# Kernel optimization log

Hardware: AMD Instinct MI355X
Metric: run time of the kernel (lower is better)

Reference implementation:

```python
import jax, jax.numpy as jnp
import numpy as np
import math

B, S, D, H, DFF, E, TOPK = 2, 2048, 768, 12, 3072, 8, 2
DH = D // H
EPS = 1e-5


def _ln(x, g, b):
    mu = jnp.mean(x, axis=-1, keepdims=True)
    var = jnp.mean(jnp.square(x - mu), axis=-1, keepdims=True)
    return (x - mu) * jax.lax.rsqrt(var + EPS) * g + b


def _router(x, rw, rb):
    # x: [B,S,D] -> probs [B,S,E], topk indices [B,S,K]
    logits = jnp.einsum('bsd,de->bse', x, rw) + rb
    probs = jax.nn.softmax(logits, axis=-1)
    topv, topi = jax.lax.top_k(probs, TOPK)
    return probs, topv, topi


def setup_inputs() -> dict:
    key = jax.random.key(0)
    ks = jax.random.split(key, 12)
    s = 0.02
    inp = {
        'x': jax.random.normal(ks[0], (B, S, D), dtype=jnp.float32),
        'wq': jax.random.normal(ks[1], (D, D), dtype=jnp.float32) * s,
        'bq': jnp.zeros((D,), jnp.float32),
        'wk': jax.random.normal(ks[2], (D, D), dtype=jnp.float32) * s,
        'bk': jnp.zeros((D,), jnp.float32),
        'wv': jax.random.normal(ks[3], (D, D), dtype=jnp.float32) * s,
        'bv': jnp.zeros((D,), jnp.float32),
        'wo': jax.random.normal(ks[4], (D, D), dtype=jnp.float32) * s,
        'bo': jnp.zeros((D,), jnp.float32),
        'norm1_g': jnp.ones((D,), jnp.float32),
        'norm1_b': jnp.zeros((D,), jnp.float32),
        'router_w': jax.random.normal(ks[5], (D, E), dtype=jnp.float32) * s,
        'router_b': jnp.zeros((E,), jnp.float32),
        'ew1': jax.random.normal(ks[6], (E, D, DFF), dtype=jnp.float32) * s,
        'eb1': jnp.zeros((E, DFF), jnp.float32),
        'ew2': jax.random.normal(ks[7], (E, DFF, D), dtype=jnp.float32) * s,
        'eb2': jnp.zeros((E, D), jnp.float32),
        'norm2_g': jnp.ones((D,), jnp.float32),
        'norm2_b': jnp.zeros((D,), jnp.float32),
    }
    return inp


def reference(x, wq, bq, wk, bk, wv, bv, wo, bo,
              norm1_g, norm1_b, router_w, router_b,
              ew1, eb1, ew2, eb2, norm2_g, norm2_b):
    # ---- multi-head self-attention ----
    def proj(w, b):
        return (jnp.einsum('bsd,de->bse', x, w) + b).reshape(B, S, H, DH).transpose(0, 2, 1, 3)
    q, k, v = proj(wq, bq), proj(wk, bk), proj(wv, bv)
    scores = jnp.einsum('bhqd,bhkd->bhqk', q, k) / math.sqrt(DH)
    attn = jax.nn.softmax(scores, axis=-1)
    ctx = jnp.einsum('bhqk,bhkd->bhqd', attn, v).transpose(0, 2, 1, 3).reshape(B, S, D)
    attn_out = jnp.einsum('bsd,de->bse', ctx, wo) + bo
    x1 = _ln(x + attn_out, norm1_g, norm1_b)

    # ---- MoE: top-k routing with renormalized gates ----
    probs, topv, topi = _router(x1, router_w, router_b)
    gates = topv / jnp.sum(topv, axis=-1, keepdims=True)          # [B,S,K]
    # combine weights per expert: [B,S,E]
    combine = jnp.sum(jax.nn.one_hot(topi, E, dtype=x1.dtype) * gates[..., None], axis=-2)
    moe_out = jnp.zeros_like(x1)
    for e in range(E):  # fixed small expert count
        h = jax.nn.relu(jnp.einsum('bsd,df->bsf', x1, ew1[e]) + eb1[e])
        y = jnp.einsum('bsf,fd->bsd', h, ew2[e]) + eb2[e]
        moe_out = moe_out + combine[..., e:e + 1] * y
    x2 = _ln(x1 + moe_out, norm2_g, norm2_b)

    # ---- redundant second router call + load-balancing aux loss ----
    probs2, _, topi2 = _router(x2, router_w, router_b)
    mask2 = jax.nn.one_hot(topi2, E, dtype=x2.dtype)              # [B,S,K,E]
    frac = jnp.mean(mask2, axis=(0, 1, 2))                        # fraction routed per expert
    prob = jnp.mean(probs2, axis=(0, 1))                          # mean router prob per expert
    aux_loss = E * jnp.sum(frac * prob)
    return (x2, aux_loss)
```

## Files before the change

### kernel.cpp

```cpp
#include <hip/hip_runtime.h>

typedef _Float16 f16;
typedef _Float16 f16x8 __attribute__((ext_vector_type(8)));
typedef _Float16 f16x4v __attribute__((ext_vector_type(4)));
typedef float f32x4 __attribute__((ext_vector_type(4)));

#define THREADS 256
#define BM 128
#define BN 128
#define BKK 64

#define WSCALE 256.0f
#define WDESCALE (1.0f/256.0f)

static __device__ __forceinline__ float wred_sum(float x){
#pragma unroll
  for (int o = 32; o; o >>= 1) x += __shfl_xor(x, o);
  return x;
}
static __device__ __forceinline__ int wred_sumi(int x){
#pragma unroll
  for (int o = 32; o; o >>= 1) x += __shfl_xor(x, o);
  return x;
}
static __device__ __forceinline__ float bred_sum(float x){
  __shared__ float r[4];
  x = wred_sum(x);
  if ((threadIdx.x & 63) == 0) r[threadIdx.x >> 6] = x;
  __syncthreads();
  float s = r[0] + r[1] + r[2] + r[3];
  __syncthreads();
  return s;
}

template<class Epi>
static __device__ __forceinline__ void gemm_core(const f16* A, const f16* BT,
                                                 int m0, int K, int N, int n0, Epi epi)
{
  __shared__ __align__(16) f16 Al[BM][BKK];
  __shared__ __align__(16) f16 Bl[BN][BKK];
  const int t = threadIdx.x;
  const int lane = t & 63, wave = t >> 6;
  const int wr = wave >> 1, wc = wave & 1;

  const f16* gA[4];
  const f16* gB[4];
#pragma unroll
  for (int i = 0; i < 4; ++i) {
    int c = i * THREADS + t;
    int r = c >> 3;
    int kc = (((c & 7) ^ (r & 7)) << 3);
    gA[i] = A + (size_t)(m0 + r) * K + kc;
    gB[i] = BT + (size_t)(n0 + r) * K + kc;
  }

  f32x4 acc[4][4];
#pragma unroll
  for (int i = 0; i < 4; ++i)
#pragma unroll
    for (int j = 0; j < 4; ++j)
#pragma unroll
      for (int r = 0; r < 4; ++r) acc[i][j][r] = 0.0f;

  f16* Als = &Al[0][0];
  f16* Bls = &Bl[0][0];

  for (int k0 = 0; k0 < K; k0 += BKK) {
    __syncthreads();
#pragma unroll
    for (int i = 0; i < 4; ++i) {
      int c = i * THREADS + t;
      __builtin_amdgcn_global_load_lds(
          (const __attribute__((address_space(1))) void*)(gA[i] + k0),
          (__attribute__((address_space(3))) void*)(Als + (size_t)c * 8), 16, 0, 0);
      __builtin_amdgcn_global_load_lds(
          (const __attribute__((address_space(1))) void*)(gB[i] + k0),
          (__attribute__((address_space(3))) void*)(Bls + (size_t)c * 8), 16, 0, 0);
    }
    __syncthreads();
#pragma unroll
    for (int kk = 0; kk < BKK; kk += 32) {
      const int lrow = lane & 15, lk = (lane >> 4) * 8;
      const int sx = (lrow & 7) << 3;
      f16x8 af[4], bf[4];
#pragma unroll
      for (int mf = 0; mf < 4; ++mf)
        af[mf] = *(const f16x8*)&Als[(size_t)(wr * 64 + mf * 16 + lrow) * BKK + ((kk + lk) ^ sx)];
#pragma unroll
      for (int nf = 0; nf < 4; ++nf)
        bf[nf] = *(const f16x8*)&Bls[(size_t)(wc * 64 + nf * 16 + lrow) * BKK + ((kk + lk) ^ sx)];
#pragma unroll
      for (int mf = 0; mf < 4; ++mf)
#pragma unroll
        for (int nf = 0; nf < 4; ++nf)
          acc[mf][nf] = __builtin_amdgcn_mfma_f32_16x16x32_f16(af[mf], bf[nf], acc[mf][nf], 0, 0, 0);
    }
  }
  const int lr4 = (lane >> 4) * 4, lc = lane & 15;
#pragma unroll
  for (int mf = 0; mf < 4; ++mf)
#pragma unroll
    for (int nf = 0; nf < 4; ++nf)
#pragma unroll
      for (int r = 0; r < 4; ++r) {
        int row = wr * 64 + mf * 16 + lr4 + r;
        int col = n0 + wc * 64 + nf * 16 + lc;
        epi(row, col, acc[mf][nf][r]);
      }
}

__global__ __launch_bounds__(256) void k_cvt(const float* x, f16* o){
  size_t i = (size_t)blockIdx.x * 256 + threadIdx.x;
  float4 v = ((const float4*)x)[i];
  f16x4v h;
  h[0] = (f16)v.x; h[1] = (f16)v.y; h[2] = (f16)v.z; h[3] = (f16)v.w;
  *(f16x4v*)(o + i * 4) = h;
}

__global__ __launch_bounds__(256) void k_transpose(const float* in, f16* out, int Kd, int Nd){
  __shared__ float tl[64][65];
  const float* ip = in + (size_t)blockIdx.z * Kd * Nd;
  f16* op = out + (size_t)blockIdx.z * Kd * Nd;
  int n0 = blockIdx.x * 64, k0 = blockIdx.y * 64;
  int tx = threadIdx.x & 15, ty = threadIdx.x >> 4;
#pragma unroll
  for (int j = 0; j < 64; j += 16) {
    float4 v = *(const float4*)(ip + (size_t)(k0 + ty + j) * Nd + n0 + tx * 4);
    tl[ty + j][tx * 4 + 0] = v.x;
    tl[ty + j][tx * 4 + 1] = v.y;
    tl[ty + j][tx * 4 + 2] = v.z;
    tl[ty + j][tx * 4 + 3] = v.w;
  }
  __syncthreads();
#pragma unroll
  for (int j = 0; j < 64; j += 16) {
    f16x4v h;
    h[0] = (f16)(tl[tx * 4 + 0][ty + j] * WSCALE);
    h[1] = (f16)(tl[tx * 4 + 1][ty + j] * WSCALE);
    h[2] = (f16)(tl[tx * 4 + 2][ty + j] * WSCALE);
    h[3] = (f16)(tl[tx * 4 + 3][ty + j] * WSCALE);
    *(f16x4v*)(op + (size_t)(n0 + ty + j) * Kd + k0 + tx * 4) = h;
  }
}

__global__ __launch_bounds__(256) void k_gemm_qkv(const f16* xb,
    const f16* wqT, const f16* wkT, const f16* wvT,
    const float* bq, const float* bk, const float* bv,
    f16* Q, f16* Ko, f16* V)
{
  int m0 = blockIdx.x * 128, n0 = blockIdx.y * 128, z = blockIdx.z;
  const f16* BT = (z == 0) ? wqT : ((z == 1) ? wkT : wvT);
  const float* bias = (z == 0) ? bq : ((z == 1) ? bk : bv);
  auto epi = [&](int row, int col, float vv) {
    int grow = m0 + row;
    int b = grow >> 11, s = grow & 2047;
    int h = col >> 6, dh = col & 63;
    float val = vv * WDESCALE + bias[col];
    if (z == 2) V[(((size_t)b * 12 + h) * 64 + dh) * 2048 + s] = (f16)val;
    else ((z == 0) ? Q : Ko)[(((size_t)b * 12 + h) * 2048 + s) * 64 + dh] = (f16)val;
  };
  gemm_core(xb, BT, m0, 768, 768, n0, epi);
}

__global__ __launch_bounds__(256, 4) void k_fattn(const f16* Qf, const f16* Kf,
                                                  const f16* Vf, float* Opart, float* lpart)
{
  __shared__ __align__(16) f16 Kl[64][72];
  __shared__ __align__(16) f16 Vl[64][72];
  __shared__ __align__(16) f16 Pl[64][72];
  const int t = threadIdx.x, lane = t & 63, wid = t >> 6;
  const int lc = lane & 15, g = lane >> 4;
  const int q0 = blockIdx.x * 64, bh = blockIdx.y, sp = blockIdx.z;
  const f16* Qh = Qf + (size_t)bh * 2048 * 64;
  const f16* Kh = Kf + ((size_t)bh * 2048 + sp * 1024) * 64;
  const f16* Vh = Vf + (size_t)bh * 64 * 2048 + sp * 1024;

  const float C1 = 0.125f * 1.44269504f;
  const float C2 = 9.0f - 2.0f * 1.44269504f;

  f16x8 aq[2];
#pragma unroll
  for (int kk = 0; kk < 2; ++kk)
    aq[kk] = *(const f16x8*)(Qh + (size_t)(q0 + wid * 16 + lc) * 64 + kk * 32 + g * 8);

  f32x4 acco[4];
  float l_[4];
#pragma unroll
  for (int nf = 0; nf < 4; ++nf)
#pragma unroll
    for (int r = 0; r < 4; ++r) acco[nf][r] = 0.f;
#pragma unroll
  for (int r = 0; r < 4; ++r) l_[r] = 0.f;

  f16x8 sk[2], sv[2];
#pragma unroll
  for (int i = 0; i < 2; ++i) {
    int c = i * 256 + t;
    sk[i] = *(const f16x8*)(Kh + (size_t)(c >> 3) * 64 + (c & 7) * 8);
    sv[i] = *(const f16x8*)(Vh + (size_t)(c >> 3) * 2048 + (c & 7) * 8);
  }

  for (int j = 0; j < 16; ++j) {
    __syncthreads();
#pragma unroll
    for (int i = 0; i < 2; ++i) {
      int c = i * 256 + t;
      *(f16x8*)&Kl[c >> 3][(c & 7) * 8] = sk[i];
      *(f16x8*)&Vl[c >> 3][(c & 7) * 8] = sv[i];
    }
    __syncthreads();

    if (j < 15) {
      const int kv1 = (j + 1) * 64;
#pragma unroll
      for (int i = 0; i < 2; ++i) {
        int c = i * 256 + t;
        sk[i] = *(const f16x8*)(Kh + (size_t)(kv1 + (c >> 3)) * 64 + (c & 7) * 8);
        sv[i] = *(const f16x8*)(Vh + (size_t)(c >> 3) * 2048 + kv1 + (c & 7) * 8);
      }
    }

    f32x4 acc[4];
#pragma unroll
    for (int nf = 0; nf < 4; ++nf)
#pragma unroll
      for (int r = 0; r < 4; ++r) acc[nf][r] = 0.f;
#pragma unroll
    for (int kk = 0; kk < 2; ++kk) {
      f16x8 bk[4];
#pragma unroll
      for (int nf = 0; nf < 4; ++nf) bk[nf] = *(const f16x8*)&Kl[nf * 16 + lc][kk * 32 + g * 8];
#pragma unroll
      for (int nf = 0; nf < 4; ++nf)
        acc[nf] = __builtin_amdgcn_mfma_f32_16x16x32_f16(aq[kk], bk[nf], acc[nf], 0, 0, 0);
    }

    {
      const int prow = wid * 16 + g * 4;
#pragma unroll
      for (int r = 0; r < 4; ++r) {
        float ls = 0.f;
#pragma unroll
        for (int nf = 0; nf < 4; ++nf) {
          float p = exp2f(fmaf(acc[nf][r], C1, C2));
          Pl[prow + r][nf * 16 + lc] = (f16)p;
          ls += p;
        }
        l_[r] += ls;
      }
    }

#pragma unroll
    for (int kk = 0; kk < 2; ++kk) {
      f16x8 ap, bv[4];
      ap = *(const f16x8*)&Pl[wid * 16 + lc][kk * 32 + g * 8];
#pragma unroll
      for (int nf = 0; nf < 4; ++nf) bv[nf] = *(const f16x8*)&Vl[nf * 16 + lc][kk * 32 + g * 8];
#pragma unroll
      for (int nf = 0; nf < 4; ++nf)
        acco[nf] = __builtin_amdgcn_mfma_f32_16x16x32_f16(ap, bv[nf], acco[nf], 0, 0, 0);
    }
  }

  float* Op = Opart + ((size_t)(sp * 24 + bh) * 2048 + q0) * 64;
  float* lp = lpart + (size_t)(sp * 24 + bh) * 2048 + q0;
#pragma unroll
  for (int r = 0; r < 4; ++r) {
    float lr = l_[r];
#pragma unroll
    for (int o = 1; o < 16; o <<= 1) lr += __shfl_xor(lr, o);
    if (lc == 0) lp[wid * 16 + g * 4 + r] = lr;
#pragma unroll
    for (int nf = 0; nf < 4; ++nf)
      Op[(size_t)(wid * 16 + g * 4 + r) * 64 + nf * 16 + lc] = acco[nf][r];
  }
}

__global__ __launch_bounds__(256) void k_attcomb(const float* Opart, const float* lpart, f16* ctx){
  size_t base = ((size_t)blockIdx.x * 256 + threadIdx.x) * 4;
  size_t row = base >> 6; int dh = base & 63;
  int bh = (int)(row >> 11), qr = (int)(row & 2047);
  int b = bh / 12, h = bh - b * 12;
  const float4 o0 = *(const float4*)(Opart + base);
  const float4 o1 = *(const float4*)(Opart + base + (size_t)24 * 2048 * 64);
  float inv = 1.f / (lpart[row] + lpart[row + 24 * 2048]);
  f16x4v hv;
  hv[0] = (f16)((o0.x + o1.x) * inv);
  hv[1] = (f16)((o0.y + o1.y) * inv);
  hv[2] = (f16)((o0.z + o1.z) * inv);
  hv[3] = (f16)((o0.w + o1.w) * inv);
  *(f16x4v*)(ctx + ((size_t)b * 2048 + qr) * 768 + h * 64 + dh) = hv;
}

__global__ __launch_bounds__(256) void k_gemm_oproj(const f16* ctx, const f16* woT,
    const float* bo, const float* x, float* x1pre)
{
  int m0 = blockIdx.x * 128, n0 = blockIdx.y * 128;
  auto epi = [&](int row, int col, float vv) {
    size_t i = (size_t)(m0 + row) * 768 + col;
    x1pre[i] = x[i] + vv * WDESCALE + bo[col];
  };
  gemm_core(ctx, woT, m0, 768, 768, n0, epi);
}

__global__ __launch_bounds__(256) void k_ln(const float* in, const float* add,
    const float* g, const float* b, float* outf, f16* outh)
{
  size_t row = blockIdx.x;
  int t = threadIdx.x;
  const float* p = in + row * 768;
  float v[3];
  float s = 0.f;
#pragma unroll
  for (int i = 0; i < 3; ++i) {
    float xv = p[t + i * 256];
    if (add) xv += add[row * 768 + t + i * 256];
    v[i] = xv; s += xv;
  }
  float mu = bred_sum(s) * (1.f / 768.f);
  float q = 0.f;
#pragma unroll
  for (int i = 0; i < 3; ++i) { float d = v[i] - mu; q += d * d; }
  float var = bred_sum(q) * (1.f / 768.f);
  float inv = rsqrtf(var + 1e-5f);
#pragma unroll
  for (int i = 0; i < 3; ++i) {
    int c = t + i * 256;
    float y = (v[i] - mu) * inv * g[c] + b[c];
    outf[row * 768 + c] = y;
    if (outh) outh[row * 768 + c] = (f16)y;
  }
}

__global__ __launch_bounds__(256) void k_ln_moe(const float* x1, const f16* ys,
    const int* inv_map, const float* gates, const float* g, const float* b, float* outf)
{
  size_t row = blockIdx.x;
  int t = threadIdx.x;
  int sl0 = inv_map[row * 2], sl1 = inv_map[row * 2 + 1];
  float g0 = gates[row * 2], g1 = gates[row * 2 + 1];
  const float* p = x1 + row * 768;
  const f16* y0 = ys + (size_t)sl0 * 768;
  const f16* y1 = ys + (size_t)sl1 * 768;
  float v[3];
  float s = 0.f;
#pragma unroll
  for (int i = 0; i < 3; ++i) {
    int c = t + i * 256;
    float xv = p[c] + g0 * (float)y0[c] + g1 * (float)y1[c];
    v[i] = xv; s += xv;
  }
  float mu = bred_sum(s) * (1.f / 768.f);
  float q = 0.f;
#pragma unroll
  for (int i = 0; i < 3; ++i) { float d = v[i] - mu; q += d * d; }
  float var = bred_sum(q) * (1.f / 768.f);
  float inv = rsqrtf(var + 1e-5f);
#pragma unroll
  for (int i = 0; i < 3; ++i) {
    int c = t + i * 256;
    outf[row * 768 + c] = (v[i] - mu) * inv * g[c] + b[c];
  }
}

__global__ __launch_bounds__(256) void k_router(const float* X, const float* rw, const float* rb,
    int* topi, float* gates, float* pprob_part, int* pcnt_part, int mode)
{
  __shared__ float sp[4][8];
  __shared__ int   si[4][2];
  int wave = threadIdx.x >> 6;
  int tok = blockIdx.x * 4 + wave;
  int lane = threadIdx.x & 63;
  const float* xr = X + (size_t)tok * 768;
  float a0=0,a1=0,a2=0,a3=0,a4=0,a5=0,a6=0,a7=0;
#pragma unroll
  for (int i = 0; i < 12; ++i) {
    int d = lane + i * 64;
    float xv = xr[d];
    float4 w0 = *(const float4*)(rw + d * 8);
    float4 w1 = *(const float4*)(rw + d * 8 + 4);
    a0 += xv*w0.x; a1 += xv*w0.y; a2 += xv*w0.z; a3 += xv*w0.w;
    a4 += xv*w1.x; a5 += xv*w1.y; a6 += xv*w1.z; a7 += xv*w1.w;
  }
  a0=wred_sum(a0); a1=wred_sum(a1); a2=wred_sum(a2); a3=wred_sum(a3);
  a4=wred_sum(a4); a5=wred_sum(a5); a6=wred_sum(a6); a7=wred_sum(a7);
  if (lane == 0) {
    float lg[8] = {a0+rb[0],a1+rb[1],a2+rb[2],a3+rb[3],a4+rb[4],a5+rb[5],a6+rb[6],a7+rb[7]};
    float mx = lg[0];
    for (int e = 1; e < 8; ++e) mx = fmaxf(mx, lg[e]);
    float pp[8], ssum = 0.f;
    for (int e = 0; e < 8; ++e) { pp[e] = expf(lg[e] - mx); ssum += pp[e]; }
    float invs = 1.f / ssum;
    for (int e = 0; e < 8; ++e) pp[e] *= invs;
    int i1 = 0; float p1 = pp[0];
    for (int e = 1; e < 8; ++e) if (pp[e] > p1) { p1 = pp[e]; i1 = e; }
    int i2 = -1; float p2 = -1.f;
    for (int e = 0; e < 8; ++e) if (e != i1 && pp[e] > p2) { p2 = pp[e]; i2 = e; }
    if (mode == 1) {
      float gs = 1.f / (p1 + p2);
      topi[tok*2] = i1; topi[tok*2+1] = i2;
      gates[tok*2] = p1*gs; gates[tok*2+1] = p2*gs;
    } else {
      for (int e = 0; e < 8; ++e) sp[wave][e] = pp[e];
      si[wave][0] = i1; si[wave][1] = i2;
    }
  }
  if (mode == 2) {
    __syncthreads();
    int t = threadIdx.x;
    if (t < 8) {
      float s = sp[0][t] + sp[1][t] + sp[2][t] + sp[3][t];
      int c = 0;
#pragma unroll
      for (int w = 0; w < 4; ++w) c += (si[w][0] == t) + (si[w][1] == t);
      pprob_part[blockIdx.x * 8 + t] = s;
      pcnt_part[blockIdx.x * 8 + t] = c;
    }
  }
}

__global__ __launch_bounds__(256) void k_plan(const int* topi, int* offal,
    int* tile_e, int* tile_r0, int* tile_e2, int* tile_r02)
{
  __shared__ int hist[8];
  int t = threadIdx.x, lane = t & 63;
  if (t < 8) hist[t] = 0;
  __syncthreads();
  int loc[8] = {0,0,0,0,0,0,0,0};
  for (int i = t; i < 8192; i += 256) ++loc[topi[i]];
#pragma unroll
  for (int e = 0; e < 8; ++e) {
    int s = wred_sumi(loc[e]);
    if (lane == 0) atomicAdd(&hist[e], s);
  }
  __syncthreads();
  if (t == 0) {
    int off = 0, t1 = 0, t2 = 0;
    for (int e = 0; e < 8; ++e) {
      offal[e] = off;
      int nt = (hist[e] + 255) >> 8;
      for (int i = 0; i < nt; ++i) {
        tile_e[t1] = e; tile_r0[t1] = off + i * 256; ++t1;
        tile_e2[t2] = e; tile_r02[t2] = off + i * 256; ++t2;
        tile_e2[t2] = e; tile_r02[t2] = off + i * 256 + 128; ++t2;
      }
      off += nt << 8;
    }
    for (; t1 < 40; ++t1) { tile_e[t1] = -1; tile_r0[t1] = 0; }
    for (; t2 < 80; ++t2) { tile_e2[t2] = -1; tile_r02[t2] = 0; }
  }
}

__global__ __launch_bounds__(512) void k_scatter(const int* topi, const float* gates,
    const int* offal, int* perm, float* gate_s, int* inv_map)
{
  int w = threadIdx.x >> 6, lane = threadIdx.x & 63;
  int base = offal[w];
  for (int it = 0; it < 128; ++it) {
    int i = it * 64 + lane;
    int e = topi[i];
    bool act = (e == w);
    unsigned long long mask = __ballot(act);
    if (act) {
      int pos = base + __popcll(mask & ((1ull << lane) - 1ull));
      perm[pos] = i >> 1;
      gate_s[pos] = gates[i];
      inv_map[i] = pos;
    }
    base += __popcll(mask);
  }
}

__global__ __launch_bounds__(512, 1) void k_gemm_moe1(const f16* x1b, const f16* ew1T,
    const float* eb1, const int* tile_e, const int* tile_r0, const int* perm, f16* hbuf)
{
  __shared__ __align__(16) f16 Al[2][256][64];
  __shared__ __align__(16) f16 Bl[2][256][64];
  int e = tile_e[blockIdx.x];
  if (e < 0) return;
  int s0 = tile_r0[blockIdx.x];
  int n0 = blockIdx.y * 256;
  const f16* BT = ew1T + (size_t)e * 3072 * 768 + (size_t)n0 * 768;
  const float* be = eb1 + e * 3072;

  const int t = threadIdx.x;
  const int lane = t & 63, wave = t >> 6;
  const int wr = wave >> 2, wc = wave & 3;

  const f16* gA[4];
  const f16* gB[4];
#pragma unroll
  for (int i = 0; i < 4; ++i) {
    int c = i * 512 + t;
    int r = c >> 3;
    int kc = (((c & 7) ^ (r & 7)) << 3);
    gA[i] = x1b + (size_t)perm[s0 + r] * 768 + kc;
    gB[i] = BT + (size_t)r * 768 + kc;
  }

  f32x4 acc[8][4];
#pragma unroll
  for (int i = 0; i < 8; ++i)
#pragma unroll
    for (int j = 0; j < 4; ++j)
#pragma unroll
      for (int r = 0; r < 4; ++r) acc[i][j][r] = 0.0f;

  auto stage = [&](int buf, int k0) {
    f16* Ad = &Al[buf][0][0];
    f16* Bd = &Bl[buf][0][0];
#pragma unroll
    for (int i = 0; i < 4; ++i) {
      int c = i * 512 + t;
      __builtin_amdgcn_global_load_lds(
          (const __attribute__((address_space(1))) void*)(gA[i] + k0),
          (__attribute__((address_space(3))) void*)(Ad + (size_t)c * 8), 16, 0, 0);
      __builtin_amdgcn_global_load_lds(
          (const __attribute__((address_space(1))) void*)(gB[i] + k0),
          (__attribute__((address_space(3))) void*)(Bd + (size_t)c * 8), 16, 0, 0);
    }
  };

  stage(0, 0);
  stage(1, 64);

  for (int ks = 0; ks < 12; ++ks) {
    const int cur = ks & 1;
    if (ks < 11) asm volatile("s_waitcnt vmcnt(8)" ::: "memory");
    else         asm volatile("s_waitcnt vmcnt(0)" ::: "memory");
    __builtin_amdgcn_s_barrier();
    asm volatile("" ::: "memory");

    const f16* Ab = &Al[cur][0][0];
    const f16* Bb = &Bl[cur][0][0];
#pragma unroll
    for (int kk = 0; kk < 64; kk += 32) {
      const int lrow = lane & 15, lk = (lane >> 4) * 8;
      const int sx = (lrow & 7) << 3;
      f16x8 af[8], bf[4];
#pragma unroll
      for (int mf = 0; mf < 8; ++mf)
        af[mf] = *(const f16x8*)&Ab[(size_t)(wr * 128 + mf * 16 + lrow) * 64 + ((kk + lk) ^ sx)];
#pragma unroll
      for (int nf = 0; nf < 4; ++nf)
        bf[nf] = *(const f16x8*)&Bb[(size_t)(wc * 64 + nf * 16 + lrow) * 64 + ((kk + lk) ^ sx)];
#pragma unroll
      for (int mf = 0; mf < 8; ++mf)
#pragma unroll
        for (int nf = 0; nf < 4; ++nf)
          acc[mf][nf] = __builtin_amdgcn_mfma_f32_16x16x32_f16(af[mf], bf[nf], acc[mf][nf], 0, 0, 0);
    }

    asm volatile("" ::: "memory");
    __builtin_amdgcn_s_barrier();
    asm volatile("" ::: "memory");
    if (ks < 10) stage(cur, (ks + 2) * 64);
  }

  const int lr4 = (lane >> 4) * 4, lc = lane & 15;
#pragma unroll
  for (int mf = 0; mf < 8; ++mf)
#pragma unroll
    for (int nf = 0; nf < 4; ++nf)
#pragma unroll
      for (int r = 0; r < 4; ++r) {
        int row = wr * 128 + mf * 16 + lr4 + r;
        int col = n0 + wc * 64 + nf * 16 + lc;
        hbuf[(size_t)(s0 + row) * 3072 + col] = (f16)fmaxf(acc[mf][nf][r] * WDESCALE + be[col], 0.f);
      }
}

__global__ __launch_bounds__(256) void k_gemm_moe2(const f16* hbuf, const f16* ew2T,
    const float* eb2, const int* tile_e2, const int* tile_r02, f16* yslots)
{
  int e = tile_e2[blockIdx.x];
  if (e < 0) return;
  int s0 = tile_r02[blockIdx.x];
  int n0 = blockIdx.y * 128;
  const f16* A = hbuf + (size_t)s0 * 3072;
  const f16* BT = ew2T + (size_t)e * 768 * 3072;
  const float* be = eb2 + e * 768;
  auto epi = [&](int row, int col, float vv) {
    yslots[(size_t)(s0 + row) * 768 + col] = (f16)(vv * WDESCALE + be[col]);
  };
  gemm_core(A, BT, 0, 3072, 768, n0, epi);
}

__global__ __launch_bounds__(256) void k_final(const float* pprob, const int* pcnt, float* out){
  __shared__ float sp[256];
  __shared__ int sc[256];
  int t = threadIdx.x, e = t & 7, g = t >> 3;
  float s = 0.f; int c = 0;
  for (int b = g; b < 1024; b += 32) { s += pprob[b * 8 + e]; c += pcnt[b * 8 + e]; }
  sp[t] = s; sc[t] = c;
  __syncthreads();
  if (t < 8) {
    float ss = 0.f; int cc = 0;
    for (int g2 = 0; g2 < 32; ++g2) { ss += sp[t + g2 * 8]; cc += sc[t + g2 * 8]; }
    sp[t] = ss; sc[t] = cc;
  }
  __syncthreads();
  if (t == 0) {
    float a = 0.f;
    for (int e2 = 0; e2 < 8; ++e2)
      a += ((float)sc[e2] * (1.f / 8192.f)) * (sp[e2] * (1.f / 4096.f));
    out[(size_t)4096 * 768] = 8.f * a;
  }
}

extern "C" void kernel_launch(void* const* d_in, const int* in_sizes, int n_in,
                              void* d_out, int out_size, void* d_ws, size_t ws_size,
                              hipStream_t stream)
{
  const float* x   = (const float*)d_in[0];
  const float* wq  = (const float*)d_in[1];
  const float* bq  = (const float*)d_in[2];
  const float* wk  = (const float*)d_in[3];
  const float* bk  = (const float*)d_in[4];
  const float* wv  = (const float*)d_in[5];
  const float* bv  = (const float*)d_in[6];
  const float* wo  = (const float*)d_in[7];
  const float* bo  = (const float*)d_in[8];
  const float* n1g = (const float*)d_in[9];
  const float* n1b = (const float*)d_in[10];
  const float* rw  = (const float*)d_in[11];
  const float* rb  = (const float*)d_in[12];
  const float* ew1 = (const float*)d_in[13];
  const float* eb1 = (const float*)d_in[14];
  const float* ew2 = (const float*)d_in[15];
  const float* eb2 = (const float*)d_in[16];
  const float* n2g = (const float*)d_in[17];
  const float* n2b = (const float*)d_in[18];
  float* out = (float*)d_out;
  char* ws = (char*)d_ws;

  size_t oWQT,oWKT,oWVT,oWOT,oEW1T,oEW2T,oXB,oQ,oK,oV,oCTX,oX1,oX1B,oYS;
  size_t oTOPI,oGATES,oOFF,oTE,oTR,oTE2,oTR2,oPERM,oGS,oINV,oH,oPP,oPC,oOP,oLP;

  {
    size_t off = 0;
    auto al = [&](size_t bytes) { size_t o = off; off += (bytes + 255) & ~(size_t)255; return o; };
    oWQT = al((size_t)768*768*2); oWKT = al((size_t)768*768*2);
    oWVT = al((size_t)768*768*2); oWOT = al((size_t)768*768*2);
    oEW1T = al((size_t)8*768*3072*2); oEW2T = al((size_t)8*768*3072*2);
    oXB  = al((size_t)4096*768*2);
    oQ   = al((size_t)24*2048*64*2); oK = al((size_t)24*2048*64*2); oV = al((size_t)24*2048*64*2);
    oCTX = al((size_t)4096*768*2);
    oX1  = al((size_t)4096*768*4);
    oX1B = al((size_t)4096*768*2);
    oYS  = al((size_t)10240*768*2);
    oTOPI = al(4096*2*4); oGATES = al(4096*2*4);
    oOFF = al(256);
    oTE = al(256); oTR = al(256); oTE2 = al(512); oTR2 = al(512);
    oPERM = al(10240*4); oGS = al(10240*4); oINV = al(8192*4);
    oH = al((size_t)10240*3072*2);
    oPP = al(1024*8*4); oPC = al(1024*8*4);
    oOP = al((size_t)2*24*2048*64*4);
    oLP = al((size_t)2*24*2048*4);
    (void)ws_size;
  }

  f16* wqT  = (f16*)(ws + oWQT);
  f16* wkT  = (f16*)(ws + oWKT);
  f16* wvT  = (f16*)(ws + oWVT);
  f16* woT  = (f16*)(ws + oWOT);
  f16* ew1T = (f16*)(ws + oEW1T);
  f16* ew2T = (f16*)(ws + oEW2T);
  f16* xb   = (f16*)(ws + oXB);
  f16* Qf   = (f16*)(ws + oQ);
  f16* Kf   = (f16*)(ws + oK);
  f16* Vf   = (f16*)(ws + oV);
  f16* ctxb = (f16*)(ws + oCTX);
  float* x1 = (float*)(ws + oX1);
  f16* x1bb = (f16*)(ws + oX1B);
  f16* yslots = (f16*)(ws + oYS);
  int* topi = (int*)(ws + oTOPI);
  float* gates = (float*)(ws + oGATES);
  int* offal  = (int*)(ws + oOFF);
  int* tile_e = (int*)(ws + oTE);
  int* tile_r0= (int*)(ws + oTR);
  int* tile_e2 = (int*)(ws + oTE2);
  int* tile_r02= (int*)(ws + oTR2);
  int* perm   = (int*)(ws + oPERM);
  float* gate_s = (float*)(ws + oGS);
  int* inv_map = (int*)(ws + oINV);
  f16* hbuf   = (f16*)(ws + oH);
  float* pprob = (float*)(ws + oPP);
  int* pcnt   = (int*)(ws + oPC);
  float* Opart = (float*)(ws + oOP);
  float* lpart = (float*)(ws + oLP);

  (void)in_sizes; (void)n_in; (void)out_size;

  hipMemsetAsync(ws + oPERM, 0, 2 * 10240 * 4, stream);

  k_cvt<<<3072, 256, 0, stream>>>(x, xb);
  k_transpose<<<dim3(12,12,1), 256, 0, stream>>>(wq, wqT, 768, 768);
  k_transpose<<<dim3(12,12,1), 256, 0, stream>>>(wk, wkT, 768, 768);
  k_transpose<<<dim3(12,12,1), 256, 0, stream>>>(wv, wvT, 768, 768);
  k_transpose<<<dim3(12,12,1), 256, 0, stream>>>(wo, woT, 768, 768);
  k_transpose<<<dim3(48,12,8), 256, 0, stream>>>(ew1, ew1T, 768, 3072);
  k_transpose<<<dim3(12,48,8), 256, 0, stream>>>(ew2, ew2T, 3072, 768);

  k_gemm_qkv<<<dim3(32,6,3), 256, 0, stream>>>(xb, wqT, wkT, wvT, bq, bk, bv, Qf, Kf, Vf);
  k_fattn<<<dim3(32,24,2), 256, 0, stream>>>(Qf, Kf, Vf, Opart, lpart);
  k_attcomb<<<3072, 256, 0, stream>>>(Opart, lpart, ctxb);
  k_gemm_oproj<<<dim3(32,6), 256, 0, stream>>>(ctxb, woT, bo, x, x1);
  k_ln<<<4096, 256, 0, stream>>>(x1, nullptr, n1g, n1b, x1, x1bb);

  k_router<<<1024, 256, 0, stream>>>(x1, rw, rb, topi, gates, pprob, pcnt, 1);
  k_plan<<<1, 256, 0, stream>>>(topi, offal, tile_e, tile_r0, tile_e2, tile_r02);
  k_scatter<<<1, 512, 0, stream>>>(topi, gates, offal, perm, gate_s, inv_map);
  k_gemm_moe1<<<dim3(40,12), 512, 0, stream>>>(x1bb, ew1T, eb1, tile_e, tile_r0, perm, hbuf);
  k_gemm_moe2<<<dim3(80,6), 256, 0, stream>>>(hbuf, ew2T, eb2, tile_e2, tile_r02, yslots);

  k_ln_moe<<<4096, 256, 0, stream>>>(x1, yslots, inv_map, gates, n2g, n2b, out);
  k_router<<<1024, 256, 0, stream>>>(out, rw, rb, topi, gates, pprob, pcnt, 2);
  k_final<<<1, 256, 0, stream>>>(pprob, pcnt, out);
}
```

Before: 434.4 us.

## Split MoE down-projection into 64-row tiles with dedicated LDS-direct GEMM kernel

The second expert GEMM (hidden→model dim, K=3072) now uses 64x128 output tiles instead of 128x128. The plan kernel emits twice as many tiles, and the launch grid doubles to 160x6. A custom kernel body replaces the shared gemm_core, loading A and B via global_load_lds into XOR-swizzled LDS and issuing 16x16x32 MFMAs. The aim is more blocks for the 256 CUs on this skinny-N, long-K GEMM, at the cost of lower reuse of the B operand per block, more B traffic, and no double-buffering in the K loop.

```diff
diff --git a/kernel.cpp b/kernel.cpp
--- a/kernel.cpp
+++ b/kernel.cpp
@@ -441,13 +441,14 @@
       int nt = (hist[e] + 255) >> 8;
       for (int i = 0; i < nt; ++i) {
         tile_e[t1] = e; tile_r0[t1] = off + i * 256; ++t1;
-        tile_e2[t2] = e; tile_r02[t2] = off + i * 256; ++t2;
-        tile_e2[t2] = e; tile_r02[t2] = off + i * 256 + 128; ++t2;
+        for (int q = 0; q < 4; ++q) {
+          tile_e2[t2] = e; tile_r02[t2] = off + i * 256 + q * 64; ++t2;
+        }
       }
       off += nt << 8;
     }
     for (; t1 < 40; ++t1) { tile_e[t1] = -1; tile_r0[t1] = 0; }
-    for (; t2 < 80; ++t2) { tile_e2[t2] = -1; tile_r02[t2] = 0; }
+    for (; t2 < 160; ++t2) { tile_e2[t2] = -1; tile_r02[t2] = 0; }
   }
 }
 
@@ -573,17 +574,94 @@
 __global__ __launch_bounds__(256) void k_gemm_moe2(const f16* hbuf, const f16* ew2T,
     const float* eb2, const int* tile_e2, const int* tile_r02, f16* yslots)
 {
+  __shared__ __align__(16) f16 Al[64][64];
+  __shared__ __align__(16) f16 Bl[128][64];
   int e = tile_e2[blockIdx.x];
   if (e < 0) return;
   int s0 = tile_r02[blockIdx.x];
   int n0 = blockIdx.y * 128;
-  const f16* A = hbuf + (size_t)s0 * 3072;
-  const f16* BT = ew2T + (size_t)e * 768 * 3072;
+  const f16* A  = hbuf + (size_t)s0 * 3072;
+  const f16* BT = ew2T + (size_t)e * 768 * 3072 + (size_t)n0 * 3072;
   const float* be = eb2 + e * 768;
-  auto epi = [&](int row, int col, float vv) {
-    yslots[(size_t)(s0 + row) * 768 + col] = (f16)(vv * WDESCALE + be[col]);
-  };
-  gemm_core(A, BT, 0, 3072, 768, n0, epi);
+
+  const int t = threadIdx.x;
+  const int lane = t & 63, wave = t >> 6;
+  const int wr = wave >> 1, wc = wave & 1;
+
+  const f16* gA[2];
+  const f16* gB[4];
+#pragma unroll
+  for (int i = 0; i < 2; ++i) {
+    int c = i * 256 + t;
+    int r = c >> 3;
+    int kc = (((c & 7) ^ (r & 7)) << 3);
+    gA[i] = A + (size_t)r * 3072 + kc;
+  }
+#pragma unroll
+  for (int i = 0; i < 4; ++i) {
+    int c = i * 256 + t;
+    int r = c >> 3;
+    int kc = (((c & 7) ^ (r & 7)) << 3);
+    gB[i] = BT + (size_t)r * 3072 + kc;
+  }
+
+  f32x4 acc[2][4];
+#pragma unroll
+  for (int i = 0; i < 2; ++i)
+#pragma unroll
+    for (int j = 0; j < 4; ++j)
+#pragma unroll
+      for (int r = 0; r < 4; ++r) acc[i][j][r] = 0.0f;
+
+  f16* Als = &Al[0][0];
+  f16* Bls = &Bl[0][0];
+
+  for (int k0 = 0; k0 < 3072; k0 += 64) {
+    __syncthreads();
+#pragma unroll
+    for (int i = 0; i < 2; ++i) {
+      int c = i * 256 + t;
+      __builtin_amdgcn_global_load_lds(
+          (const __attribute__((address_space(1))) void*)(gA[i] + k0),
+          (__attribute__((address_space(3))) void*)(Als + (size_t)c * 8), 16, 0, 0);
+    }
+#pragma unroll
+    for (int i = 0; i < 4; ++i) {
+      int c = i * 256 + t;
+      __builtin_amdgcn_global_load_lds(
+          (const __attribute__((address_space(1))) void*)(gB[i] + k0),
+          (__attribute__((address_space(3))) void*)(Bls + (size_t)c * 8), 16, 0, 0);
+    }
+    __syncthreads();
+#pragma unroll
+    for (int kk = 0; kk < 64; kk += 32) {
+      const int lrow = lane & 15, lk = (lane >> 4) * 8;
+      const int sx = (lrow & 7) << 3;
+      f16x8 af[2], bf[4];
+#pragma unroll
+      for (int mf = 0; mf < 2; ++mf)
+        af[mf] = *(const f16x8*)&Als[(size_t)(wr * 32 + mf * 16 + lrow) * 64 + ((kk + lk) ^ sx)];
+#pragma unroll
+      for (int nf = 0; nf < 4; ++nf)
+        bf[nf] = *(const f16x8*)&Bls[(size_t)(wc * 64 + nf * 16 + lrow) * 64 + ((kk + lk) ^ sx)];
+#pragma unroll
+      for (int mf = 0; mf < 2; ++mf)
+#pragma unroll
+        for (int nf = 0; nf < 4; ++nf)
+          acc[mf][nf] = __builtin_amdgcn_mfma_f32_16x16x32_f16(af[mf], bf[nf], acc[mf][nf], 0, 0, 0);
+    }
+  }
+  const int lr4 = (lane >> 4) * 4, lc = lane & 15;
+#pragma unroll
+  for (int mf = 0; mf < 2; ++mf)
+#pragma unroll
+    for (int nf = 0; nf < 4; ++nf)
+#pragma unroll
+      for (int r = 0; r < 4; ++r) {
+        int row = wr * 32 + mf * 16 + lr4 + r;
+        int col = n0 + wc * 64 + nf * 16 + lc;
+        yslots[(size_t)(s0 + row) * 768 + col] = (f16)(acc[mf][nf][r] * WDESCALE + be[col]);
+      }
 }
 
 __global__ __launch_bounds__(256) void k_final(const float* pprob, const int* pcnt, float* out){
@@ -651,7 +729,7 @@
     oYS  = al((size_t)10240*768*2);
     oTOPI = al(4096*2*4); oGATES = al(4096*2*4);
     oOFF = al(256);
-    oTE = al(256); oTR = al(256); oTE2 = al(512); oTR2 = al(512);
+    oTE = al(256); oTR = al(256); oTE2 = al(1024); oTR2 = al(1024);
     oPERM = al(10240*4); oGS = al(10240*4); oINV = al(8192*4);
     oH = al((size_t)10240*3072*2);
     oPP = al(1024*8*4); oPC = al(1024*8*4);
@@ -712,7 +790,7 @@
   k_plan<<<1, 256, 0, stream>>>(topi, offal, tile_e, tile_r0, tile_e2, tile_r02);
   k_scatter<<<1, 512, 0, stream>>>(topi, gates, offal, perm, gate_s, inv_map);
   k_gemm_moe1<<<dim3(40,12), 512, 0, stream>>>(x1bb, ew1T, eb1, tile_e, tile_r0, perm, hbuf);
-  k_gemm_moe2<<<dim3(80,6), 256, 0, stream>>>(hbuf, ew2T, eb2, tile_e2, tile_r02, yslots);
+  k_gemm_moe2<<<dim3(160,6), 256, 0, stream>>>(hbuf, ew2T, eb2, tile_e2, tile_r02, yslots);
 
   k_ln_moe<<<4096, 256, 0, stream>>>(x1, yslots, inv_map, gates, n2g, n2b, out);
   k_router<<<1024, 256, 0, stream>>>(out, rw, rb, topi, gates, pprob, pcnt, 2);
```

Result: slower. 458.2 us (+5.5%).
